# Performance work log

Hardware: AMD Instinct MI355X
Metric: run time of the kernel (lower is better)

The kernel has to match this reference:

```python
import jax, jax.numpy as jnp
import numpy as np

B, N, C, H, P = 8, 4096, 512, 8, 64
D = C // H


def setup_inputs() -> dict:
    key = jax.random.key(0)
    ks = jax.random.split(key, 5)
    s = 0.02
    return {
        "x": jax.random.normal(ks[0], (B, N, C), jnp.float32),
        "w_qkv": jax.random.normal(ks[1], (3 * C, C), jnp.float32) * s,
        "w_e": jax.random.normal(ks[2], (P, N), jnp.float32) * s,
        "b_e": jnp.zeros((P,), jnp.float32),
        "temperature": jnp.ones((1, 1, 1), jnp.float32),
        "temperature2": jnp.ones((H, 1, 1), jnp.float32),
        "w_o1": jax.random.normal(ks[3], (C // 2, C), jnp.float32) * s,
        "b_o1": jnp.zeros((C // 2,), jnp.float32),
        "w_o2": jax.random.normal(ks[4], (C // 2, C), jnp.float32) * s,
        "b_o2": jnp.zeros((C // 2,), jnp.float32),
    }


def reference(x, w_qkv, w_e, b_e, temperature, temperature2, w_o1, b_o1, w_o2, b_o2):
    Bs, Ns, Cs = x.shape
    # qkvv projection and head split: [B,N,3C] -> [3,B,H,N,D]
    qkv = (x @ w_qkv.T).reshape(Bs, Ns, 3, H, D)
    qkv = jnp.transpose(qkv, (2, 0, 3, 1, 4))
    q, k, v = qkv[0], qkv[1], qkv[2]
    q_t = jnp.swapaxes(q, -2, -1)  # [B,H,D,N]
    k_t = jnp.swapaxes(k, -2, -1)  # [B,H,D,N]
    v_t = jnp.swapaxes(v, -2, -1)  # [B,H,D,N]
    # Linformer-style projection along token axis; E = F (shared weights)
    kp = k_t @ w_e.T + b_e  # [B,H,D,P]
    vp = v_t @ w_e.T + b_e  # [B,H,D,P]
    # L2-normalize q along tokens (k is normalized in the original AFTER
    # projection, so that normalization is dead code and omitted)
    qn = q_t / jnp.maximum(jnp.linalg.norm(q_t, axis=-1, keepdims=True), 1e-12)
    # ---- channel attention: [B,C,C] scores over raw x ----
    xt = jnp.swapaxes(x, -2, -1)  # [B,C,N]
    attn_ca = jax.nn.softmax((xt @ x) * temperature, axis=-1)
    x_ca = jnp.swapaxes(attn_ca @ xt, -2, -1)  # [B,N,C]
    # ---- projected spatial attention: [B,H,N,P] scores ----
    attn_sa = jax.nn.softmax(
        jnp.einsum('bhdn,bhdp->bhnp', qn, kp) * temperature2, axis=-1)
    x_sa = jnp.einsum('bhnp,bhdp->bhnd', attn_sa, vp)  # [B,H,N,D]
    # faithful to torch: permute(0,3,1,2) then reshape(B,N,C)
    x_sa = jnp.transpose(x_sa, (0, 3, 1, 2)).reshape(Bs, Ns, Cs)
    out = jnp.concatenate(
        [x_sa @ w_o1.T + b_o1, x_ca @ w_o2.T + b_o2], axis=-1)
    return out
```

## Files before the change

kernel.cpp:

```cpp
#include <hip/hip_runtime.h>
#include <hip/hip_bf16.h>

typedef unsigned short u16;

#define AS1 __attribute__((address_space(1)))
#define AS3 __attribute__((address_space(3)))

static __device__ __forceinline__ float bl(u16 v) {
    return __uint_as_float(((unsigned)v) << 16);
}
static __device__ __forceinline__ u16 f2b(float f) {
    unsigned u = __float_as_uint(f);
    unsigned r = u + 0x7FFFu + ((u >> 16) & 1u);
    return (u16)(r >> 16);
}
static __device__ __forceinline__ float ldf(const void* p, long i, int isbf) {
    if (isbf) return bl(((const u16*)p)[i]);
    return ((const float*)p)[i];
}
static __device__ __forceinline__ void gload_lds16(const u16* g, u16* l) {
    __builtin_amdgcn_global_load_lds((const AS1 void*)g, (AS3 void*)l, 16, 0, 0);
}

typedef __attribute__((ext_vector_type(8))) short bf16x8;
typedef __attribute__((ext_vector_type(4))) float f32x4;

static __device__ __forceinline__ bf16x8 pack8(const float* p) {
    const float4 x0 = ((const float4*)p)[0];
    const float4 x1 = ((const float4*)p)[1];
    unsigned r0, r1, r2, r3;
    asm("v_cvt_pk_bf16_f32 %0, %1, %2" : "=v"(r0) : "v"(x0.x), "v"(x0.y));
    asm("v_cvt_pk_bf16_f32 %0, %1, %2" : "=v"(r1) : "v"(x0.z), "v"(x0.w));
    asm("v_cvt_pk_bf16_f32 %0, %1, %2" : "=v"(r2) : "v"(x1.x), "v"(x1.y));
    asm("v_cvt_pk_bf16_f32 %0, %1, %2" : "=v"(r3) : "v"(x1.z), "v"(x1.w));
    union { unsigned u[4]; bf16x8 v; } u;
    u.u[0] = r0; u.u[1] = r1; u.u[2] = r2; u.u[3] = r3;
    return u.v;
}

__global__ void dtype_probe(const void* __restrict__ temp, unsigned* __restrict__ flag) {
    if (threadIdx.x == 0 && blockIdx.x == 0)
        flag[0] = (((const u16*)temp)[0] == 0x3F80) ? 1u : 0u;
}

__global__ __launch_bounds__(256) void zero_f32(float* __restrict__ p, long n) {
    const long stride = (long)gridDim.x * 256;
    for (long i = (long)blockIdx.x * 256 + threadIdx.x; i < n; i += stride)
        p[i] = 0.f;
}

__global__ __launch_bounds__(256) void conv_x(const void* __restrict__ X,
                                              u16* __restrict__ xb,
                                              u16* __restrict__ xt,
                                              const unsigned* __restrict__ flg)
{
    __shared__ u16 tile[64][65];
    const int f = (int)flg[0];
    const int b = blockIdx.z;
    const int n0 = blockIdx.x * 64, c0 = blockIdx.y * 64;
    const int t = threadIdx.x, r0 = t >> 6, c = t & 63;
    #pragma unroll
    for (int rr = 0; rr < 16; ++rr) {
        const int r = rr * 4 + r0;
        const long gi = ((long)b * 4096 + n0 + r) * 512 + c0 + c;
        const u16 h = f2b(ldf(X, gi, f));
        xb[gi] = h;
        tile[r][c] = h;
    }
    __syncthreads();
    #pragma unroll
    for (int rr = 0; rr < 16; ++rr) {
        const int cc = rr * 4 + r0;
        xt[((long)b * 512 + c0 + cc) * 4096 + n0 + c] = tile[c][cc];
    }
}

__global__ __launch_bounds__(256) void conv_w(const void* __restrict__ W,
                                              u16* __restrict__ wb, long nelem,
                                              const unsigned* __restrict__ flg)
{
    const int f = (int)flg[0];
    const long stride = (long)gridDim.x * 256;
    for (long i = (long)blockIdx.x * 256 + threadIdx.x; i < nelem; i += stride)
        wb[i] = f2b(ldf(W, i, f));
}

__global__ __launch_bounds__(512, 2) void gemm256_nt(
    const u16* __restrict__ A, const u16* __restrict__ B,
    void* __restrict__ C, const void* __restrict__ bias,
    int K, int lda, int ldb, int ldc,
    long sA, long sB, long sC,
    const unsigned* __restrict__ flg, int biasExt, int cF32,
    float* __restrict__ qsq,
    const u16* __restrict__ A2, const u16* __restrict__ B2,
    const void* __restrict__ bias2, int nSwitch, long sB2)
{
    __shared__ u16 Asm[2][256 * 32];
    __shared__ u16 Bsm[2][256 * 32];
    const int t = threadIdx.x, w = t >> 6, l = t & 63;
    const int gx = gridDim.x, gy = gridDim.y;
    const long nwg = (long)gx * gy * gridDim.z;
    const long lin = blockIdx.x + (long)gx * (blockIdx.y + (long)gy * blockIdx.z);
    long nid = lin;
    if ((nwg & 7) == 0) nid = (lin & 7) * (nwg >> 3) + (lin >> 3);
    const int by = (int)(nid % gy);
    const long r2 = nid / gy;
    const int bx = (int)(r2 % gx);
    const int bz = (int)(r2 / gx);
    const int m0 = bx * 256, n0 = by * 256;
    const u16* Asel = A; const u16* Bsel = B; const void* bsel = bias;
    long sBv = sB;
    int nLoc = n0;
    if (A2 && n0 >= nSwitch) { Asel = A2; Bsel = B2; bsel = bias2; nLoc = n0 - nSwitch; sBv = sB2; }
    const u16* Ab = Asel + (long)bz * sA;
    const u16* Bb = Bsel + (long)bz * sBv + (long)nLoc * ldb;
    const int wm = (w >> 1) * 64, wn = (w & 1) * 128;
    const int srow = l >> 2;
    const int selem = (((l & 3) ^ (srow & 3)) << 3);
    const int fr = l & 15;
    const int fk = (l >> 4) * 8;
    const int xorv = (fr & 3) << 3;
    f32x4 acc[4][8];
    #pragma unroll
    for (int i = 0; i < 4; ++i)
        #pragma unroll
        for (int j = 0; j < 8; ++j)
            acc[i][j] = (f32x4){0.f, 0.f, 0.f, 0.f};

#define STAGE256(nb, kk)                                                                     \
    do {                                                                                     \
        gload_lds16(Ab + (long)(m0 + w * 16 + srow) * lda + (kk) + selem, &Asm[nb][w * 512]);        \
        gload_lds16(Ab + (long)(m0 + (w + 8) * 16 + srow) * lda + (kk) + selem, &Asm[nb][(w + 8) * 512]); \
        gload_lds16(Bb + (long)(w * 16 + srow) * ldb + (kk) + selem, &Bsm[nb][w * 512]);             \
        gload_lds16(Bb + (long)((w + 8) * 16 + srow) * ldb + (kk) + selem, &Bsm[nb][(w + 8) * 512]);     \
    } while (0)

    STAGE256(0, 0);
    __syncthreads();
    int cur = 0;
    for (int k0 = 0; k0 < K; k0 += 32) {
        if (k0 + 32 < K) STAGE256(cur ^ 1, k0 + 32);
        bf16x8 af[4], bf[8];
        #pragma unroll
        for (int i = 0; i < 4; ++i)
            af[i] = *(const bf16x8*)&Asm[cur][((wm + i * 16 + fr) << 5) + (fk ^ xorv)];
        #pragma unroll
        for (int j = 0; j < 8; ++j)
            bf[j] = *(const bf16x8*)&Bsm[cur][((wn + j * 16 + fr) << 5) + (fk ^ xorv)];
        #pragma unroll
        for (int i = 0; i < 4; ++i)
            #pragma unroll
            for (int j = 0; j < 8; ++j)
                acc[i][j] = __builtin_amdgcn_mfma_f32_16x16x32_bf16(af[i], bf[j], acc[i][j], 0, 0, 0);
        __syncthreads();
        cur ^= 1;
    }
#undef STAGE256

    const int f = (int)flg[0];
    const long cOff = (long)bz * sC;
    float bj[8];
    #pragma unroll
    for (int j = 0; j < 8; ++j) bj[j] = 0.f;
    if (bsel) {
        #pragma unroll
        for (int j = 0; j < 8; ++j)
            bj[j] = ldf(bsel, (nLoc & 255) + wn + j * 16 + fr, biasExt ? f : 1);
    }
    #pragma unroll
    for (int i = 0; i < 4; ++i) {
        #pragma unroll
        for (int j = 0; j < 8; ++j) {
            const int col = n0 + wn + j * 16 + fr;
            #pragma unroll
            for (int r = 0; r < 4; ++r) {
                const int row = m0 + wm + i * 16 + (l >> 4) * 4 + r;
                const float v = acc[i][j][r] + bj[j];
                if (cF32) ((float*)C)[cOff + (long)row * ldc + col] = v;
                else      ((u16*)C)[cOff + (long)row * ldc + col] = f2b(v);
            }
        }
    }
    if (qsq) {
        #pragma unroll
        for (int j = 0; j < 8; ++j) {
            const int col = n0 + wn + j * 16 + fr;
            if (col < 512) {
                float s = 0.f;
                #pragma unroll
                for (int i = 0; i < 4; ++i)
                    #pragma unroll
                    for (int r = 0; r < 4; ++r)
                        s = fmaf(acc[i][j][r], acc[i][j][r], s);
                s += __shfl_xor(s, 16, 64);
                s += __shfl_xor(s, 32, 64);
                if ((l >> 4) == 0)
                    atomicAdd(&qsq[(long)bz * 512 + col], s);
            }
        }
    }
}

__global__ __launch_bounds__(256) void gram128_sym(
    const u16* __restrict__ XT, float* __restrict__ SP)
{
    __shared__ u16 Asm[2][128 * 32];
    __shared__ u16 Bsm[2][128 * 32];
    const int t = threadIdx.x, w = t >> 6, l = t & 63;
    const int tx = blockIdx.x, b = blockIdx.y, kz = blockIdx.z;
    int ti, tj;
    if (tx < 4)      { ti = 0; tj = tx; }
    else if (tx < 7) { ti = 1; tj = tx - 3; }
    else if (tx < 9) { ti = 2; tj = tx - 5; }
    else             { ti = 3; tj = 3; }
    const int diag = (ti == tj);
    const int m0 = ti * 128, n0 = tj * 128;
    const u16* Ab = XT + (long)b * 512 * 4096 + (long)m0 * 4096;
    const u16* Bb = XT + (long)b * 512 * 4096 + (long)n0 * 4096;
    const int wm = (w >> 1) * 64, wn = (w & 1) * 64;
    const int srow = l >> 2;
    const int scol = (l & 3) * 8;
    const int fr = l & 15;
    const int fk = (l >> 4) * 8;
    f32x4 acc[4][4];
    #pragma unroll
    for (int i = 0; i < 4; ++i)
        #pragma unroll
        for (int j = 0; j < 4; ++j)
            acc[i][j] = (f32x4){0.f, 0.f, 0.f, 0.f};

    const int q0 = w, q1 = w + 4;
#define GSTAGE(nb, kk)                                                                  \
    do {                                                                                \
        gload_lds16(Ab + (long)(q0 * 16 + srow) * 4096 + (kk) + scol, &Asm[nb][q0 * 512]);      \
        gload_lds16(Ab + (long)(q1 * 16 + srow) * 4096 + (kk) + scol, &Asm[nb][q1 * 512]);      \
        if (!diag) {                                                                    \
            gload_lds16(Bb + (long)(q0 * 16 + srow) * 4096 + (kk) + scol, &Bsm[nb][q0 * 512]);  \
            gload_lds16(Bb + (long)(q1 * 16 + srow) * 4096 + (kk) + scol, &Bsm[nb][q1 * 512]);  \
        }                                                                               \
    } while (0)

    const int kBeg = kz * 512, kEnd = kBeg + 512;
    GSTAGE(0, kBeg);
    __syncthreads();
    int cur = 0;
    for (int k0 = kBeg; k0 < kEnd; k0 += 32) {
        if (k0 + 32 < kEnd) GSTAGE(cur ^ 1, k0 + 32);
        const u16* Bsrc = diag ? &Asm[cur][0] : &Bsm[cur][0];
        bf16x8 af[4], bf[4];
        #pragma unroll
        for (int i = 0; i < 4; ++i) {
            af[i] = *(const bf16x8*)&Asm[cur][(wm + i * 16 + fr) * 32 + fk];
            bf[i] = *(const bf16x8*)&Bsrc[(wn + i * 16 + fr) * 32 + fk];
        }
        #pragma unroll
        for (int i = 0; i < 4; ++i)
            #pragma unroll
            for (int j = 0; j < 4; ++j)
                acc[i][j] = __builtin_amdgcn_mfma_f32_16x16x32_bf16(af[i], bf[j], acc[i][j], 0, 0, 0);
        __syncthreads();
        cur ^= 1;
    }
#undef GSTAGE

    float* Sb = SP + ((long)kz * 8 + b) * 262144;
    #pragma unroll
    for (int i = 0; i < 4; ++i) {
        #pragma unroll
        for (int j = 0; j < 4; ++j) {
            const int col = n0 + wn + j * 16 + fr;
            #pragma unroll
            for (int r = 0; r < 4; ++r) {
                const int row = m0 + wm + i * 16 + (l >> 4) * 4 + r;
                const float v = acc[i][j][r];
                Sb[(long)row * 512 + col] = v;
                if (!diag) Sb[(long)col * 512 + row] = v;
            }
        }
    }
}

__global__ __launch_bounds__(256) void m2_gemm(const u16* __restrict__ WO2,
                                               const u16* __restrict__ ATTN,
                                               u16* __restrict__ M2)
{
    __shared__ u16 Asm[128 * 32];
    __shared__ u16 Bsm[128 * 48];
    const int t = threadIdx.x, w = t >> 6, l = t & 63;
    const int m0 = blockIdx.x * 128, n0 = blockIdx.y * 128, b = blockIdx.z;
    const u16* At = ATTN + (long)b * 262144;
    const int wm = (w >> 1) * 64, wn = (w & 1) * 64;
    const int srow = l >> 2, scol = (l & 3) * 8;
    const int fr = l & 15, fk = (l >> 4) * 8;
    const int br = t >> 3;
    const int bc = (t & 7) * 16;
    f32x4 acc[4][4];
    #pragma unroll
    for (int i = 0; i < 4; ++i)
        #pragma unroll
        for (int j = 0; j < 4; ++j)
            acc[i][j] = (f32x4){0.f, 0.f, 0.f, 0.f};

    for (int k0 = 0; k0 < 512; k0 += 32) {
        __syncthreads();
        gload_lds16(WO2 + (long)(m0 + w * 16 + srow) * 512 + k0 + scol, &Asm[w * 512]);
        gload_lds16(WO2 + (long)(m0 + (w + 4) * 16 + srow) * 512 + k0 + scol, &Asm[(w + 4) * 512]);
        {
            const u16* src = At + (long)(k0 + br) * 512 + n0 + bc;
            u16 tmp[16];
            #pragma unroll
            for (int i = 0; i < 16; ++i) tmp[i] = src[i];
            #pragma unroll
            for (int i = 0; i < 16; ++i) Bsm[(bc + i) * 48 + br] = tmp[i];
        }
        __syncthreads();
        bf16x8 af[4], bf[4];
        #pragma unroll
        for (int i = 0; i < 4; ++i) {
            af[i] = *(const bf16x8*)&Asm[(wm + i * 16 + fr) * 32 + fk];
            bf[i] = *(const bf16x8*)&Bsm[(wn + i * 16 + fr) * 48 + fk];
        }
        #pragma unroll
        for (int i = 0; i < 4; ++i)
            #pragma unroll
            for (int j = 0; j < 4; ++j)
                acc[i][j] = __builtin_amdgcn_mfma_f32_16x16x32_bf16(af[i], bf[j], acc[i][j], 0, 0, 0);
    }

    u16* Mb = M2 + (long)b * 131072;
    #pragma unroll
    for (int i = 0; i < 4; ++i) {
        #pragma unroll
        for (int j = 0; j < 4; ++j) {
            const int col = n0 + wn + j * 16 + fr;
            #pragma unroll
            for (int r = 0; r < 4; ++r) {
                const int row = m0 + wm + i * 16 + (l >> 4) * 4 + r;
                Mb[(long)row * 512 + col] = f2b(acc[i][j][r]);
            }
        }
    }
}

__global__ __launch_bounds__(256) void xe_mfma(const u16* __restrict__ WEB,
                                               const u16* __restrict__ XT,
                                               float* __restrict__ XE)
{
    const int t = threadIdx.x, w = t >> 6, l = t & 63;
    const int l15 = l & 15, g = l >> 4;
    const int c0 = blockIdx.x * 128 + (w >> 1) * 64;
    const int b = blockIdx.y;
    const int nbase = blockIdx.z * 512 + (w & 1) * 256;
    f32x4 acc[4][4];
    #pragma unroll
    for (int i = 0; i < 4; ++i)
        #pragma unroll
        for (int j = 0; j < 4; ++j)
            acc[i][j] = (f32x4){0.f, 0.f, 0.f, 0.f};
    for (int ks = 0; ks < 8; ++ks) {
        const int n = nbase + ks * 32 + g * 8;
        bf16x8 a[4], bb[4];
        #pragma unroll
        for (int i = 0; i < 4; ++i)
            a[i] = *(const bf16x8*)&WEB[(long)(i * 16 + l15) * 4096 + n];
        #pragma unroll
        for (int j = 0; j < 4; ++j)
            bb[j] = *(const bf16x8*)&XT[((long)b * 512 + c0 + j * 16 + l15) * 4096 + n];
        #pragma unroll
        for (int i = 0; i < 4; ++i)
            #pragma unroll
            for (int j = 0; j < 4; ++j)
                acc[i][j] = __builtin_amdgcn_mfma_f32_16x16x32_bf16(a[i], bb[j], acc[i][j], 0, 0, 0);
    }
    #pragma unroll
    for (int i = 0; i < 4; ++i)
        #pragma unroll
        for (int j = 0; j < 4; ++j)
            #pragma unroll
            for (int r = 0; r < 4; ++r)
                atomicAdd(&XE[((long)b * 64 + i * 16 + g * 4 + r) * 512 + c0 + j * 16 + l15],
                          acc[i][j][r]);
}

__global__ __launch_bounds__(256) void kpvp2_mfma(const float* __restrict__ XE,
                                                  const u16* __restrict__ WQB,
                                                  const float* __restrict__ qsq,
                                                  const void* __restrict__ be,
                                                  const void* __restrict__ temp2,
                                                  u16* __restrict__ kpT,
                                                  u16* __restrict__ vpB,
                                                  const unsigned* __restrict__ flg)
{
    __shared__ float lds[4][4096];
    const int bh = blockIdx.x, b = bh >> 3, h = bh & 7;
    const int t = threadIdx.x, w = t >> 6, l = t & 63;
    const int l15 = l & 15, g = l >> 4;
    const int isV = w >> 1;
    const int ch = w & 1;
    const u16* wrow = WQB + (long)(512 + isV * 512 + h * 64) * 512;
    const float* xr = XE + (long)b * 64 * 512;
    f32x4 acc[4][4];
    #pragma unroll
    for (int i = 0; i < 4; ++i)
        #pragma unroll
        for (int j = 0; j < 4; ++j)
            acc[i][j] = (f32x4){0.f, 0.f, 0.f, 0.f};
    for (int ks = 0; ks < 8; ++ks) {
        const int c = ch * 256 + ks * 32 + g * 8;
        bf16x8 a[4], bb[4];
        if (!isV) {
            #pragma unroll
            for (int i = 0; i < 4; ++i)
                a[i] = pack8(&xr[(long)(i * 16 + l15) * 512 + c]);
            #pragma unroll
            for (int j = 0; j < 4; ++j)
                bb[j] = *(const bf16x8*)&wrow[(long)(j * 16 + l15) * 512 + c];
        } else {
            #pragma unroll
            for (int i = 0; i < 4; ++i)
                a[i] = *(const bf16x8*)&wrow[(long)(i * 16 + l15) * 512 + c];
            #pragma unroll
            for (int j = 0; j < 4; ++j)
                bb[j] = pack8(&xr[(long)(j * 16 + l15) * 512 + c]);
        }
        #pragma unroll
        for (int i = 0; i < 4; ++i)
            #pragma unroll
            for (int j = 0; j < 4; ++j)
                acc[i][j] = __builtin_amdgcn_mfma_f32_16x16x32_bf16(a[i], bb[j], acc[i][j], 0, 0, 0);
    }
    #pragma unroll
    for (int i = 0; i < 4; ++i)
        #pragma unroll
        for (int j = 0; j < 4; ++j)
            #pragma unroll
            for (int r = 0; r < 4; ++r)
                lds[w][(i * 16 + g * 4 + r) * 64 + j * 16 + l15] = acc[i][j][r];
    __syncthreads();
    const int f = (int)flg[0];
    if (t < 128) {
        const float t2 = ldf(temp2, h, f);
        for (int e = t; e < 4096; e += 128) {
            const int p = e >> 6, d = e & 63;
            const float rn = 1.0f / fmaxf(sqrtf(qsq[b * 512 + h * 64 + d]), 1e-12f);
            kpT[(long)bh * 4096 + e] = f2b((lds[0][e] + lds[1][e] + ldf(be, p, f)) * rn * t2);
        }
    } else {
        for (int e = t - 128; e < 4096; e += 128) {
            vpB[(long)bh * 4096 + e] = f2b(lds[2][e] + lds[3][e] + ldf(be, e & 63, f));
        }
    }
}

__global__ __launch_bounds__(256) void softmax_ca(const float* __restrict__ SP,
                                                  u16* __restrict__ A,
                                                  const void* __restrict__ temp,
                                                  const unsigned* __restrict__ flg)
{
    __shared__ float red[256];
    const int row = blockIdx.x;
    const int t = threadIdx.x;
    const float tv = ldf(temp, 0, (int)flg[0]);
    const float* s = SP + (long)row * 512;
    const long kzs = (long)8 * 512 * 512;
    float v0 = 0.f, v1 = 0.f;
    #pragma unroll
    for (int z = 0; z < 8; ++z) {
        v0 += s[z * kzs + t];
        v1 += s[z * kzs + t + 256];
    }
    v0 *= tv;
    v1 *= tv;
    red[t] = fmaxf(v0, v1);
    __syncthreads();
    for (int o = 128; o > 0; o >>= 1) {
        if (t < o) red[t] = fmaxf(red[t], red[t + o]);
        __syncthreads();
    }
    const float m = red[0];
    __syncthreads();
    float e0 = expf(v0 - m), e1 = expf(v1 - m);
    red[t] = e0 + e1;
    __syncthreads();
    for (int o = 128; o > 0; o >>= 1) {
        if (t < o) red[t] += red[t + o];
        __syncthreads();
    }
    const float inv = 1.0f / red[0];
    u16* a = A + (long)row * 512;
    a[t]       = f2b(e0 * inv);
    a[t + 256] = f2b(e1 * inv);
}

__global__ __launch_bounds__(256) void spatial_attn_mfma(
    const u16* __restrict__ Q, const u16* __restrict__ kpT,
    const u16* __restrict__ vpB, u16* __restrict__ XSA)
{
    __shared__ u16 P[4][4096];
    const int bh = blockIdx.y, b = bh >> 3, h = bh & 7;
    const int t = threadIdx.x, w = t >> 6, l = t & 63;
    const int l15 = l & 15, g = l >> 4;
    const int n0 = blockIdx.x * 256 + w * 64;
    char* Pw = (char*)&P[w][0];

    const u16* kb = kpT + (long)bh * 4096;
    const u16* vb = vpB + (long)bh * 4096;
    bf16x8 akp[2][4], avp[2][4];
    #pragma unroll
    for (int ks = 0; ks < 2; ++ks)
        #pragma unroll
        for (int i = 0; i < 4; ++i) {
            akp[ks][i] = *(const bf16x8*)&kb[(i * 16 + l15) * 64 + ks * 32 + g * 8];
            avp[ks][i] = *(const bf16x8*)&vb[(i * 16 + l15) * 64 + ks * 32 + g * 8];
        }

    f32x4 sacc[4][4];
    #pragma unroll
    for (int i = 0; i < 4; ++i)
        #pragma unroll
        for (int j = 0; j < 4; ++j)
            sacc[i][j] = (f32x4){0.f, 0.f, 0.f, 0.f};
    const u16* qb = Q + ((long)b * 4096 + n0) * 512 + h * 64;
    #pragma unroll
    for (int ks = 0; ks < 2; ++ks) {
        bf16x8 bq[4];
        #pragma unroll
        for (int j = 0; j < 4; ++j)
            bq[j] = *(const bf16x8*)&qb[(long)(j * 16 + l15) * 512 + ks * 32 + g * 8];
        #pragma unroll
        for (int i = 0; i < 4; ++i)
            #pragma unroll
            for (int j = 0; j < 4; ++j)
                sacc[i][j] = __builtin_amdgcn_mfma_f32_16x16x32_bf16(akp[ks][i], bq[j], sacc[i][j], 0, 0, 0);
    }

    #pragma unroll
    for (int j = 0; j < 4; ++j) {
        float m = sacc[0][j][0];
        #pragma unroll
        for (int i = 0; i < 4; ++i)
            #pragma unroll
            for (int r = 0; r < 4; ++r)
                m = fmaxf(m, sacc[i][j][r]);
        m = fmaxf(m, __shfl_xor(m, 16, 64));
        m = fmaxf(m, __shfl_xor(m, 32, 64));
        float s = 0.f;
        #pragma unroll
        for (int i = 0; i < 4; ++i)
            #pragma unroll
            for (int r = 0; r < 4; ++r) {
                const float e = __expf(sacc[i][j][r] - m);
                sacc[i][j][r] = e;
                s += e;
            }
        s += __shfl_xor(s, 16, 64);
        s += __shfl_xor(s, 32, 64);
        const float inv = 1.0f / s;
        const int n = j * 16 + l15;
        const int swz = (n & 7) << 4;
        #pragma unroll
        for (int i = 0; i < 4; ++i) {
            unsigned lo, hi;
            float p0 = sacc[i][j][0] * inv, p1 = sacc[i][j][1] * inv;
            float p2 = sacc[i][j][2] * inv, p3 = sacc[i][j][3] * inv;
            asm("v_cvt_pk_bf16_f32 %0, %1, %2" : "=v"(lo) : "v"(p0), "v"(p1));
            asm("v_cvt_pk_bf16_f32 %0, %1, %2" : "=v"(hi) : "v"(p2), "v"(p3));
            const int byte = (n * 128 + i * 32 + g * 8) ^ swz;
            *(uint2*)(Pw + byte) = make_uint2(lo, hi);
        }
    }

    f32x4 oacc[4][4];
    #pragma unroll
    for (int i = 0; i < 4; ++i)
        #pragma unroll
        for (int j = 0; j < 4; ++j)
            oacc[i][j] = (f32x4){0.f, 0.f, 0.f, 0.f};
    #pragma unroll
    for (int ks = 0; ks < 2; ++ks) {
        bf16x8 bp[4];
        #pragma unroll
        for (int j = 0; j < 4; ++j) {
            const int n = j * 16 + l15;
            const int byte = (n * 128 + ks * 64 + g * 16) ^ ((n & 7) << 4);
            bp[j] = *(const bf16x8*)(Pw + byte);
        }
        #pragma unroll
        for (int i = 0; i < 4; ++i)
            #pragma unroll
            for (int j = 0; j < 4; ++j)
                oacc[i][j] = __builtin_amdgcn_mfma_f32_16x16x32_bf16(avp[ks][i], bp[j], oacc[i][j], 0, 0, 0);
    }

    const int rowoff = h * 8 + (n0 >> 9);
    const int colbase = n0 & 511;
    #pragma unroll
    for (int i = 0; i < 4; ++i)
        #pragma unroll
        for (int r = 0; r < 4; ++r) {
            const int d = i * 16 + g * 4 + r;
            u16* orow = XSA + ((long)b * 4096 + d * 64 + rowoff) * 512 + colbase;
            #pragma unroll
            for (int j = 0; j < 4; ++j)
                orow[j * 16 + l15] = f2b(oacc[i][j][r]);
        }
}

extern "C" void kernel_launch(void* const* d_in, const int* in_sizes, int n_in,
                              void* d_out, int out_size, void* d_ws, size_t ws_size,
                              hipStream_t stream)
{
    const void* x     = d_in[0];
    const void* w_qkv = d_in[1];
    const void* w_e   = d_in[2];
    const void* b_e   = d_in[3];
    const void* temp  = d_in[4];
    const void* temp2 = d_in[5];
    const void* w_o1  = d_in[6];
    const void* b_o1  = d_in[7];
    const void* w_o2  = d_in[8];
    const void* b_o2  = d_in[9];
    float* out = (float*)d_out;

    char* ws = (char*)d_ws;
    unsigned* flag = (unsigned*)ws; ws += 256;
    u16*   qb     = (u16*)ws;   ws += (size_t)8 * 4096 * 512 * 2;
    float* qsq    = (float*)ws; ws += (size_t)4096 * 4;
    float* xe     = (float*)ws; ws += (size_t)8 * 64 * 512 * 4;
    float* scpart = (float*)ws; ws += (size_t)8 * 8 * 512 * 512 * 4;
    u16*   attn   = (u16*)ws;   ws += (size_t)8 * 512 * 512 * 2;
    u16*   m2     = (u16*)ws;   ws += (size_t)8 * 256 * 512 * 2;
    u16*   xt     = (u16*)ws;   ws += (size_t)8 * 512 * 4096 * 2;
    u16*   xb     = (u16*)ws;   ws += (size_t)8 * 4096 * 512 * 2;
    u16*   wqb    = (u16*)ws;   ws += (size_t)1536 * 512 * 2;
    u16*   web    = (u16*)ws;   ws += (size_t)64 * 4096 * 2;
    u16*   wo1b   = (u16*)ws;   ws += (size_t)256 * 512 * 2;
    u16*   wo2b   = (u16*)ws;   ws += (size_t)256 * 512 * 2;
    u16*   kpT    = (u16*)ws;   ws += (size_t)262144 * 2;
    u16*   vpB    = (u16*)ws;   ws += (size_t)262144 * 2;
    u16*   x_sa   = xt;

    dtype_probe<<<1, 64, 0, stream>>>(temp, flag);
    conv_x<<<dim3(64, 8, 8), 256, 0, stream>>>(x, xb, xt, flag);
    conv_w<<<768, 256, 0, stream>>>(w_qkv, wqb, 1536L * 512, flag);
    conv_w<<<128, 256, 0, stream>>>(w_e, web, 64L * 4096, flag);
    conv_w<<<128, 256, 0, stream>>>(w_o1, wo1b, 256L * 512, flag);
    conv_w<<<128, 256, 0, stream>>>(w_o2, wo2b, 256L * 512, flag);
    zero_f32<<<4, 256, 0, stream>>>(qsq, 4096);
    gemm256_nt<<<dim3(16, 2, 8), 512, 0, stream>>>(
        xb, wqb, qb, nullptr, 512, 512, 512, 512,
        (long)4096 * 512, 0, (long)4096 * 512, flag, 0, 0, qsq,
        nullptr, nullptr, nullptr, 1 << 30, 0);
    zero_f32<<<128, 256, 0, stream>>>(xe, (long)8 * 64 * 512);
    xe_mfma<<<dim3(4, 8, 8), 256, 0, stream>>>(web, xt, xe);
    kpvp2_mfma<<<64, 256, 0, stream>>>(xe, wqb, qsq, b_e, temp2, kpT, vpB, flag);
    gram128_sym<<<dim3(10, 8, 8), 256, 0, stream>>>(xt, scpart);
    softmax_ca<<<4096, 256, 0, stream>>>(scpart, attn, temp, flag);
    m2_gemm<<<dim3(2, 4, 8), 256, 0, stream>>>(wo2b, attn, m2);
    spatial_attn_mfma<<<dim3(16, 64), 256, 0, stream>>>(qb, kpT, vpB, x_sa);
    gemm256_nt<<<dim3(16, 2, 8), 512, 0, stream>>>(
        x_sa, wo1b, out, b_o1, 512, 512, 512, 512,
        (long)4096 * 512, 0, (long)4096 * 512, flag, 1, 1, nullptr,
        xb, m2, b_o2, 256, (long)256 * 512);
}
```

Measured before the change: 374.2 us.

## Load Gram MFMA operands directly from global and halve split-K partitions

The symmetric Gram kernel no longer stages X^T tiles through double-buffered LDS with async global-to-LDS loads and barriers; each wave now reads its bf16x8 MFMA fragments straight from global memory. The split-K factor drops from 8 to 4 (1024-wide K chunks), halving the partial-score buffer that softmax_ca must sum. The aim is to remove LDS traffic and synchronization and to cut partial-sum memory writes and reads. The cost is no data sharing between waves through LDS, so global/L2 loads are duplicated, and the grid has half as many blocks, which lowers parallelism.

Result: slower. 395.7 us (+5.7%).

```diff
diff --git a/kernel.cpp b/kernel.cpp
--- a/kernel.cpp
+++ b/kernel.cpp
@@ -201,11 +201,9 @@
     }
 }
 
-__global__ __launch_bounds__(256) void gram128_sym(
+__global__ __launch_bounds__(256) void gram_direct(
     const u16* __restrict__ XT, float* __restrict__ SP)
 {
-    __shared__ u16 Asm[2][128 * 32];
-    __shared__ u16 Bsm[2][128 * 32];
     const int t = threadIdx.x, w = t >> 6, l = t & 63;
     const int tx = blockIdx.x, b = blockIdx.y, kz = blockIdx.z;
     int ti, tj;
@@ -215,13 +213,10 @@
     else             { ti = 3; tj = 3; }
     const int diag = (ti == tj);
     const int m0 = ti * 128, n0 = tj * 128;
-    const u16* Ab = XT + (long)b * 512 * 4096 + (long)m0 * 4096;
-    const u16* Bb = XT + (long)b * 512 * 4096 + (long)n0 * 4096;
     const int wm = (w >> 1) * 64, wn = (w & 1) * 64;
-    const int srow = l >> 2;
-    const int scol = (l & 3) * 8;
-    const int fr = l & 15;
-    const int fk = (l >> 4) * 8;
+    const int l15 = l & 15, g = l >> 4;
+    const u16* Ab = XT + (long)b * 512 * 4096 + (long)(m0 + wm) * 4096;
+    const u16* Bb = XT + (long)b * 512 * 4096 + (long)(n0 + wn) * 4096;
     f32x4 acc[4][4];
     #pragma unroll
     for (int i = 0; i < 4; ++i)
@@ -229,49 +224,32 @@
         for (int j = 0; j < 4; ++j)
             acc[i][j] = (f32x4){0.f, 0.f, 0.f, 0.f};
 
-    const int q0 = w, q1 = w + 4;
-#define GSTAGE(nb, kk)                                                                  \
-    do {                                                                                \
-        gload_lds16(Ab + (long)(q0 * 16 + srow) * 4096 + (kk) + scol, &Asm[nb][q0 * 512]);      \
-        gload_lds16(Ab + (long)(q1 * 16 + srow) * 4096 + (kk) + scol, &Asm[nb][q1 * 512]);      \
-        if (!diag) {                                                                    \
-            gload_lds16(Bb + (long)(q0 * 16 + srow) * 4096 + (kk) + scol, &Bsm[nb][q0 * 512]);  \
-            gload_lds16(Bb + (long)(q1 * 16 + srow) * 4096 + (kk) + scol, &Bsm[nb][q1 * 512]);  \
-        }                                                                               \
-    } while (0)
-
-    const int kBeg = kz * 512, kEnd = kBeg + 512;
-    GSTAGE(0, kBeg);
-    __syncthreads();
-    int cur = 0;
-    for (int k0 = kBeg; k0 < kEnd; k0 += 32) {
-        if (k0 + 32 < kEnd) GSTAGE(cur ^ 1, k0 + 32);
-        const u16* Bsrc = diag ? &Asm[cur][0] : &Bsm[cur][0];
-        bf16x8 af[4], bf[4];
-        #pragma unroll
-        for (int i = 0; i < 4; ++i) {
-            af[i] = *(const bf16x8*)&Asm[cur][(wm + i * 16 + fr) * 32 + fk];
-            bf[i] = *(const bf16x8*)&Bsrc[(wn + i * 16 + fr) * 32 + fk];
-        }
-        #pragma unroll
-        for (int i = 0; i < 4; ++i)
-            #pragma unroll
-            for (int j = 0; j < 4; ++j)
-                acc[i][j] = __builtin_amdgcn_mfma_f32_16x16x32_bf16(af[i], bf[j], acc[i][j], 0, 0, 0);
-        __syncthreads();
-        cur ^= 1;
-    }
-#undef GSTAGE
+    const int kBeg = kz * 1024;
+    #pragma unroll 2
+    for (int k0 = kBeg; k0 < kBeg + 1024; k0 += 32) {
+        bf16x8 a[4], bb[4];
+        #pragma unroll
+        for (int i = 0; i < 4; ++i)
+            a[i] = *(const bf16x8*)&Ab[(long)(i * 16 + l15) * 4096 + k0 + g * 8];
+        #pragma unroll
+        for (int j = 0; j < 4; ++j)
+            bb[j] = *(const bf16x8*)&Bb[(long)(j * 16 + l15) * 4096 + k0 + g * 8];
+        #pragma unroll
+        for (int i = 0; i < 4; ++i)
+            #pragma unroll
+            for (int j = 0; j < 4; ++j)
+                acc[i][j] = __builtin_amdgcn_mfma_f32_16x16x32_bf16(a[i], bb[j], acc[i][j], 0, 0, 0);
+    }
 
     float* Sb = SP + ((long)kz * 8 + b) * 262144;
     #pragma unroll
     for (int i = 0; i < 4; ++i) {
         #pragma unroll
         for (int j = 0; j < 4; ++j) {
-            const int col = n0 + wn + j * 16 + fr;
+            const int col = n0 + wn + j * 16 + l15;
             #pragma unroll
             for (int r = 0; r < 4; ++r) {
-                const int row = m0 + wm + i * 16 + (l >> 4) * 4 + r;
+                const int row = m0 + wm + i * 16 + g * 4 + r;
                 const float v = acc[i][j][r];
                 Sb[(long)row * 512 + col] = v;
                 if (!diag) Sb[(long)col * 512 + row] = v;
@@ -465,7 +443,7 @@
     const long kzs = (long)8 * 512 * 512;
     float v0 = 0.f, v1 = 0.f;
     #pragma unroll
-    for (int z = 0; z < 8; ++z) {
+    for (int z = 0; z < 4; ++z) {
         v0 += s[z * kzs + t];
         v1 += s[z * kzs + t + 256];
     }
@@ -627,7 +605,7 @@
     u16*   qb     = (u16*)ws;   ws += (size_t)8 * 4096 * 512 * 2;
     float* qsq    = (float*)ws; ws += (size_t)4096 * 4;
     float* xe     = (float*)ws; ws += (size_t)8 * 64 * 512 * 4;
-    float* scpart = (float*)ws; ws += (size_t)8 * 8 * 512 * 512 * 4;
+    float* scpart = (float*)ws; ws += (size_t)4 * 8 * 512 * 512 * 4;
     u16*   attn   = (u16*)ws;   ws += (size_t)8 * 512 * 512 * 2;
     u16*   m2     = (u16*)ws;   ws += (size_t)8 * 256 * 512 * 2;
     u16*   xt     = (u16*)ws;   ws += (size_t)8 * 512 * 4096 * 2;
@@ -654,7 +632,7 @@
     zero_f32<<<128, 256, 0, stream>>>(xe, (long)8 * 64 * 512);
     xe_mfma<<<dim3(4, 8, 8), 256, 0, stream>>>(web, xt, xe);
     kpvp2_mfma<<<64, 256, 0, stream>>>(xe, wqb, qsq, b_e, temp2, kpT, vpB, flag);
-    gram128_sym<<<dim3(10, 8, 8), 256, 0, stream>>>(xt, scpart);
+    gram_direct<<<dim3(10, 8, 4), 256, 0, stream>>>(xt, scpart);
     softmax_ca<<<4096, 256, 0, stream>>>(scpart, attn, temp, flag);
     m2_gemm<<<dim3(2, 4, 8), 256, 0, stream>>>(wo2b, attn, m2);
     spatial_attn_mfma<<<dim3(16, 64), 256, 0, stream>>>(qb, kpT, vpB, x_sa);
```
